# Kernel tuning notes

Measured on AMD Instinct MI355X. Metric: run time of the kernel, lower is better.

Reference implementation:

```python
import jax, jax.numpy as jnp
import numpy as np
from jax import lax

B, NODE, T, D_IN = 8, 1024, 12, 16
HID, GAT_OUT, PRED_LEN = 32, 32, 6
HEADS = 3
F_IN = HID * T      # 384
C = GAT_OUT * T     # 384
N = B * NODE        # 8192
E = 65536


def setup_inputs() -> dict:
    key = jax.random.key(0)
    ks = jax.random.split(key, 24)
    s = 0.05
    inp = {}
    inp["x"] = jax.random.normal(ks[0], (B, NODE, T, D_IN), jnp.float32)
    inp["edge_index"] = jax.random.randint(ks[1], (2, E), 0, N)
    inp["edge_attr"] = jax.random.normal(ks[2], (E, 1), jnp.float32)
    inp["batch_vec"] = jnp.repeat(jnp.arange(B), NODE)
    inp["alpha"] = 1.0
    # GRU params (torch gate order: r, z, n)
    inp["Wih"] = jax.random.normal(ks[3], (3 * HID, D_IN), jnp.float32) * s
    inp["Whh"] = jax.random.normal(ks[4], (3 * HID, HID), jnp.float32) * s
    inp["bih"] = jax.random.normal(ks[5], (3 * HID,), jnp.float32) * s
    inp["bhh"] = jax.random.normal(ks[6], (3 * HID,), jnp.float32) * s
    # GATConv params
    inp["Wgat"] = jax.random.normal(ks[7], (HEADS * C, F_IN), jnp.float32) * s
    inp["att_src"] = jax.random.normal(ks[8], (1, HEADS, C), jnp.float32) * s
    inp["att_dst"] = jax.random.normal(ks[9], (1, HEADS, C), jnp.float32) * s
    inp["Wedge"] = jax.random.normal(ks[10], (HEADS * C, 1), jnp.float32) * s
    inp["att_edge"] = jax.random.normal(ks[11], (1, HEADS, C), jnp.float32) * s
    inp["gat_bias"] = jax.random.normal(ks[12], (C,), jnp.float32) * s
    # predictors / classifiers
    inp["Wp1"] = jax.random.normal(ks[13], (1, GAT_OUT), jnp.float32) * s
    inp["bp1"] = jax.random.normal(ks[14], (1,), jnp.float32) * s
    inp["Wp3"] = jax.random.normal(ks[15], (PRED_LEN, T), jnp.float32) * s
    inp["bp3"] = jax.random.normal(ks[16], (PRED_LEN,), jnp.float32) * s
    inp["Wc1"] = jax.random.normal(ks[17], (GAT_OUT, T * GAT_OUT), jnp.float32) * s
    inp["bc1"] = jax.random.normal(ks[18], (GAT_OUT,), jnp.float32) * s
    inp["Wc2"] = jax.random.normal(ks[19], (2, GAT_OUT), jnp.float32) * s
    inp["bc2"] = jax.random.normal(ks[20], (2,), jnp.float32) * s
    return inp


def _gru(x, Wih, Whh, bih, bhh):
    # x: [rows, T, D_IN] -> [rows, T, HID]
    h0 = jnp.zeros((x.shape[0], HID), x.dtype)

    def step(h, xt):
        gi = xt @ Wih.T + bih
        gh = h @ Whh.T + bhh
        ir, iz, inn = jnp.split(gi, 3, axis=-1)
        hr, hz, hn = jnp.split(gh, 3, axis=-1)
        r = jax.nn.sigmoid(ir + hr)
        z = jax.nn.sigmoid(iz + hz)
        n = jnp.tanh(inn + r * hn)
        h_new = (1.0 - z) * n + z * h
        return h_new, h_new

    _, hs = lax.scan(step, h0, jnp.swapaxes(x, 0, 1))
    return jnp.swapaxes(hs, 0, 1)


def _gat(x, edge_index, edge_attr, Wgat, att_src, att_dst, Wedge, att_edge, bias):
    # PyG GATConv, heads=HEADS, concat=False, edge_dim=1, no self loops
    h = (x @ Wgat.T).reshape(N, HEADS, C)          # [N,H,C]
    a_src = (h * att_src).sum(-1)                  # [N,H]
    a_dst = (h * att_dst).sum(-1)                  # [N,H]
    src, dst = edge_index[0], edge_index[1]
    e = (edge_attr @ Wedge.T).reshape(-1, HEADS, C)
    a_edge = (e * att_edge).sum(-1)                # [E,H]
    a = jax.nn.leaky_relu(a_src[src] + a_dst[dst] + a_edge, 0.2)
    amax = jax.ops.segment_max(a, dst, num_segments=N)
    a = jnp.exp(a - amax[dst])
    denom = jax.ops.segment_sum(a, dst, num_segments=N)
    a = a / (denom[dst] + 1e-16)                   # segment softmax over incoming edges
    msg = h[src] * a[:, :, None]                   # [E,H,C]
    out = jax.ops.segment_sum(msg, dst, num_segments=N)
    return out.mean(axis=1) + bias                 # concat=False -> head mean


def reference(x, edge_index, edge_attr, batch_vec, alpha,
              Wih, Whh, bih, bhh,
              Wgat, att_src, att_dst, Wedge, att_edge, gat_bias,
              Wp1, bp1, Wp3, bp3, Wc1, bc1, Wc2, bc2):
    gru_in = x.reshape(-1, T, D_IN)                       # [N,T,D]
    gru_out = _gru(gru_in, Wih, Whh, bih, bhh)            # [N,T,HID]
    gat_in = gru_out.reshape(N, F_IN)
    gat_out = _gat(gat_in, edge_index, edge_attr, Wgat, att_src, att_dst,
                   Wedge, att_edge, gat_bias)             # [N,C]
    lin_in = gat_out.reshape(-1, T, GAT_OUT)              # [N,T,GAT_OUT]
    p = jax.nn.relu(jnp.einsum('ntc,oc->nto', lin_in, Wp1) + bp1).squeeze(-1)  # [N,T]
    p = jax.nn.relu(p @ Wp3.T + bp3)                      # [N,PRED_LEN]
    out_pred = p.reshape(B, NODE, PRED_LEN)
    # GRL is identity in forward
    pooled = jax.ops.segment_max(gat_out, batch_vec, num_segments=B)  # [B,C]
    l1 = pooled @ Wc1.T + bc1
    l2 = l1 @ Wc2.T + bc2
    out_label = jax.nn.softmax(l2, axis=1)
    return out_pred, out_label
```

## Files before the change

kernel.cpp:

```cpp
#include <hip/hip_runtime.h>
#include <hip/hip_bf16.h>

#define N_NODES 8192
#define E_EDGES 65536
#define CDIM 384
#define NHC 1152
#define T_STEPS 12
#define PRED_LEN 6
#define OUT_LABEL_OFF 49152

#define O_X        0u
#define O_WIH      1572864u
#define O_WHH      1574400u
#define O_BIH      1577472u
#define O_BHH      1577568u
#define O_WGAT     1577664u
#define O_ATTS     2020032u
#define O_ATTD     2021184u
#define O_WEDGE    2022336u
#define O_ATTE     2023488u
#define O_GBIAS    2024640u
#define O_WP1      2025024u
#define O_BP1      2025056u
#define O_WP3      2025057u
#define O_BP3      2025129u
#define O_WC1      2025135u
#define O_BC1      2037423u
#define O_WC2      2037455u
#define O_BC2      2037519u
#define O_EATTR    2037521u
#define CONV_TOTAL 2103057u

#define O_GATIN    2103072u
#define O_GATB     O_GATIN
#define O_WGATB    (O_GATIN + 1572864u)
#define O_DEG      (O_GATIN + 1794048u)
#define O_HFEAT    5248800u
#define O_ASRC     14685984u
#define O_ADST     14710560u
#define O_WEXP     14931744u
#define O_DENOM    15152928u
#define O_GMEAN    15177504u
#define O_POOLED   18323232u
#define O_KH       18326304u
#define O_FLAG     18326307u
#define O_BUCKET   18326320u

typedef __attribute__((ext_vector_type(8))) short short8;
typedef __attribute__((ext_vector_type(4))) float floatx4;

__device__ __forceinline__ float b2f(unsigned short u) {
    return __uint_as_float(((unsigned)u) << 16);
}
__device__ __forceinline__ unsigned short f2b(float f) {
    __hip_bfloat16 b = __float2bfloat16(f);
    return *(unsigned short*)&b;
}
__device__ __forceinline__ short f2bs(float f) {
    __hip_bfloat16 b = __float2bfloat16(f);
    return *(short*)&b;
}
__device__ __forceinline__ unsigned enc_f(float f) {
    unsigned u = __float_as_uint(f);
    return (u & 0x80000000u) ? ~u : (u | 0x80000000u);
}
__device__ __forceinline__ float dec_f(unsigned e) {
    return __uint_as_float((e & 0x80000000u) ? (e & 0x7FFFFFFFu) : ~e);
}
__device__ __forceinline__ float fast_rcp(float x) {
    return __builtin_amdgcn_rcpf(x);
}

__global__ __launch_bounds__(256) void prep_kernel(
    const void* Wih, const void* Whh, const void* bih, const void* bhh,
    const void* Wgat, const void* atts, const void* attd, const void* Wedge, const void* atte,
    const void* gbias, const void* Wp1, const void* bp1, const void* Wp3, const void* bp3,
    const void* Wc1, const void* bc1, const void* Wc2, const void* bc2, const void* eattr,
    float* __restrict__ W, unsigned short* __restrict__ wgatb, int* __restrict__ flag_g)
{
    __shared__ int fsh;
    if (threadIdx.x < 64) {
        int lane = threadIdx.x, cnt = 0;
#pragma unroll
        for (int i = 0; i < 8; i++) {
            unsigned short h = ((const unsigned short*)Wih)[(lane * 8 + i) * 2];
            int e = (h >> 7) & 0xFF;
            if (e >= 100 && e <= 127) cnt++;
        }
#pragma unroll
        for (int off = 32; off; off >>= 1) cnt += __shfl_down(cnt, off, 64);
        if (lane == 0) fsh = (cnt >= 300) ? 1 : 0;
    }
    __syncthreads();
    int flag = fsh;
    unsigned tidg = blockIdx.x * 256 + threadIdx.x;
    if (tidg == 0) *flag_g = flag;
    if      (tidg < 24576u) W[O_DENOM + tidg] = 0.f;
    else if (tidg < 27648u) W[O_POOLED + tidg - 24576u] = 0.f;
    else if (tidg < 35840u) ((int*)(W + O_DEG))[tidg - 27648u] = 0;
    unsigned idx = tidg + O_WIH;
    if (idx >= CONV_TOTAL) return;
    if (idx >= O_WGAT && idx < O_ATTS) {
        unsigned off = idx - O_WGAT;
        wgatb[off] = flag ? ((const unsigned short*)Wgat)[off]
                          : f2b(((const float*)Wgat)[off]);
        return;
    }
    const void* src; unsigned off;
    if      (idx < O_WHH)   { src = Wih;   off = idx - O_WIH; }
    else if (idx < O_BIH)   { src = Whh;   off = idx - O_WHH; }
    else if (idx < O_BHH)   { src = bih;   off = idx - O_BIH; }
    else if (idx < O_WGAT)  { src = bhh;   off = idx - O_BHH; }
    else if (idx < O_ATTD)  { src = atts;  off = idx - O_ATTS; }
    else if (idx < O_WEDGE) { src = attd;  off = idx - O_ATTD; }
    else if (idx < O_ATTE)  { src = Wedge; off = idx - O_WEDGE; }
    else if (idx < O_GBIAS) { src = atte;  off = idx - O_ATTE; }
    else if (idx < O_WP1)   { src = gbias; off = idx - O_GBIAS; }
    else if (idx < O_BP1)   { src = Wp1;   off = idx - O_WP1; }
    else if (idx < O_BP3)   { src = (idx == O_BP1) ? bp1 : Wp3; off = (idx == O_BP1) ? 0 : idx - O_WP3; }
    else if (idx < O_WC1)   { src = bp3;   off = idx - O_BP3; }
    else if (idx < O_BC1)   { src = Wc1;   off = idx - O_WC1; }
    else if (idx < O_WC2)   { src = bc1;   off = idx - O_BC1; }
    else if (idx < O_BC2)   { src = Wc2;   off = idx - O_WC2; }
    else if (idx < O_EATTR) { src = bc2;   off = idx - O_BC2; }
    else                    { src = eattr; off = idx - O_EATTR; }
    W[idx] = flag ? b2f(((const unsigned short*)src)[off])
                  : ((const float*)src)[off];
}

__global__ __launch_bounds__(64, 1) void gru_kernel(
    const float* __restrict__ W,
    const void* __restrict__ xraw,
    unsigned short* __restrict__ gat_b)
{
    __shared__ short hbuf[16 * 40];
    int lane = threadIdx.x;
    int q = lane >> 4, nl = lane & 15;
    int n0 = blockIdx.x * 16;
    int n = n0 + nl;
    int flag = ((const int*)(W + O_FLAG))[0];

    const float* W_wih = W + O_WIH;
    const float* W_whh = W + O_WHH;
    const float* W_bih = W + O_BIH;
    const float* W_bhh = W + O_BHH;

    short8 wh[6], wi[6];
#pragma unroll
    for (int c = 0; c < 6; c++) {
        int row = c * 16 + nl;
#pragma unroll
        for (int r = 0; r < 8; r++) {
            wh[c][r] = f2bs(W_whh[row * 32 + 8 * q + r]);
            int k = 8 * q + r;
            wi[c][r] = (k < 16) ? f2bs(W_wih[row * 16 + k]) : (short)0;
        }
    }
    float br[8], bz[8], bni[8], bnh[8];
#pragma unroll
    for (int idx = 0; idx < 8; idx++) {
        int c = idx >> 2, r = idx & 3;
        int j = c * 16 + 4 * q + r;
        br[idx]  = W_bih[j] + W_bhh[j];
        bz[idx]  = W_bih[32 + j] + W_bhh[32 + j];
        bni[idx] = W_bih[64 + j];
        bnh[idx] = W_bhh[64 + j];
    }

    floatx4 zf = {0.f, 0.f, 0.f, 0.f};
    short8 zs;
#pragma unroll
    for (int r = 0; r < 8; r++) zs[r] = 0;

    float hprev[8];
#pragma unroll
    for (int i = 0; i < 8; i++) hprev[i] = 0.f;
    short8 hfrag = zs;

    for (int t = 0; t < T_STEPS; t++) {
        short8 xf = zs;
        if (q < 2) {
            size_t xoff = (size_t)n * 192 + t * 16 + 8 * q;
            if (flag) {
                xf = *(const short8*)((const unsigned short*)xraw + xoff);
            } else {
                const float* xp = (const float*)xraw + xoff;
                float4 xa = *(const float4*)xp;
                float4 xb = *(const float4*)(xp + 4);
                xf[0] = f2bs(xa.x); xf[1] = f2bs(xa.y); xf[2] = f2bs(xa.z); xf[3] = f2bs(xa.w);
                xf[4] = f2bs(xb.x); xf[5] = f2bs(xb.y); xf[6] = f2bs(xb.z); xf[7] = f2bs(xb.w);
            }
        }

        floatx4 aR0 = __builtin_amdgcn_mfma_f32_16x16x32_bf16(wi[0], xf, zf, 0, 0, 0);
        aR0 = __builtin_amdgcn_mfma_f32_16x16x32_bf16(wh[0], hfrag, aR0, 0, 0, 0);
        floatx4 aR1 = __builtin_amdgcn_mfma_f32_16x16x32_bf16(wi[1], xf, zf, 0, 0, 0);
        aR1 = __builtin_amdgcn_mfma_f32_16x16x32_bf16(wh[1], hfrag, aR1, 0, 0, 0);
        floatx4 aZ0 = __builtin_amdgcn_mfma_f32_16x16x32_bf16(wi[2], xf, zf, 0, 0, 0);
        aZ0 = __builtin_amdgcn_mfma_f32_16x16x32_bf16(wh[2], hfrag, aZ0, 0, 0, 0);
        floatx4 aZ1 = __builtin_amdgcn_mfma_f32_16x16x32_bf16(wi[3], xf, zf, 0, 0, 0);
        aZ1 = __builtin_amdgcn_mfma_f32_16x16x32_bf16(wh[3], hfrag, aZ1, 0, 0, 0);
        floatx4 aNI0 = __builtin_amdgcn_mfma_f32_16x16x32_bf16(wi[4], xf, zf, 0, 0, 0);
        floatx4 aNI1 = __builtin_amdgcn_mfma_f32_16x16x32_bf16(wi[5], xf, zf, 0, 0, 0);
        floatx4 aNH0 = __builtin_amdgcn_mfma_f32_16x16x32_bf16(wh[4], hfrag, zf, 0, 0, 0);
        floatx4 aNH1 = __builtin_amdgcn_mfma_f32_16x16x32_bf16(wh[5], hfrag, zf, 0, 0, 0);

#pragma unroll
        for (int idx = 0; idx < 8; idx++) {
            int c = idx >> 2, r = idx & 3;
            float vR = (c ? aR1[r] : aR0[r]) + br[idx];
            float vZ = (c ? aZ1[r] : aZ0[r]) + bz[idx];
            float vNI = (c ? aNI1[r] : aNI0[r]) + bni[idx];
            float vNH = (c ? aNH1[r] : aNH0[r]) + bnh[idx];
            float rr = fast_rcp(1.f + __expf(-vR));
            float zz = fast_rcp(1.f + __expf(-vZ));
            float pre = vNI + rr * vNH;
            float e2 = __expf(2.f * pre);
            float nn = 1.f - 2.f * fast_rcp(e2 + 1.f);
            float h = (1.f - zz) * nn + zz * hprev[idx];
            hprev[idx] = h;
            int j = c * 16 + 4 * q + r;
            hbuf[nl * 40 + j] = f2bs(h);
        }
        hfrag = *(short8*)&hbuf[nl * 40 + 8 * q];
        int sn = lane >> 2, jg = (lane & 3) * 8;
        short8 hv = *(short8*)&hbuf[sn * 40 + jg];
        *(short8*)(gat_b + (size_t)(n0 + sn) * 384 + t * 32 + jg) = hv;
    }
}

__global__ __launch_bounds__(256) void gemm_mfma(
    const unsigned short* __restrict__ Ab,
    const unsigned short* __restrict__ Bb,
    unsigned short* __restrict__ Cb)
{
    __shared__ unsigned short sA[128][40];
    __shared__ unsigned short sB[128][40];
    int tid = threadIdx.x;
    int wave = tid >> 6, lane = tid & 63;
    int wm = (wave >> 1) * 64, wn = (wave & 1) * 64;
    int m0 = blockIdx.x * 128, n0 = blockIdx.y * 128;

    int r0 = tid >> 2;
    int c8 = (tid & 3) * 8;

    floatx4 acc[4][4];
#pragma unroll
    for (int i = 0; i < 4; i++)
#pragma unroll
        for (int j = 0; j < 4; j++) acc[i][j] = 0;

    int ml = lane & 15, kq = (lane >> 4) * 8;

    for (int k0 = 0; k0 < 384; k0 += 32) {
        short8 a0 = *(const short8*)(Ab + (size_t)(m0 + r0) * 384 + k0 + c8);
        short8 a1 = *(const short8*)(Ab + (size_t)(m0 + r0 + 64) * 384 + k0 + c8);
        short8 b0 = *(const short8*)(Bb + (size_t)(n0 + r0) * 384 + k0 + c8);
        short8 b1 = *(const short8*)(Bb + (size_t)(n0 + r0 + 64) * 384 + k0 + c8);

        __syncthreads();
        *(short8*)(&sA[r0][c8])      = a0;
        *(short8*)(&sA[r0 + 64][c8]) = a1;
        *(short8*)(&sB[r0][c8])      = b0;
        *(short8*)(&sB[r0 + 64][c8]) = b1;
        __syncthreads();

        short8 af[4], bf[4];
#pragma unroll
        for (int i = 0; i < 4; i++)
            af[i] = *(const short8*)(&sA[wm + i * 16 + ml][kq]);
#pragma unroll
        for (int j = 0; j < 4; j++)
            bf[j] = *(const short8*)(&sB[wn + j * 16 + ml][kq]);
#pragma unroll
        for (int i = 0; i < 4; i++)
#pragma unroll
            for (int j = 0; j < 4; j++)
                acc[i][j] = __builtin_amdgcn_mfma_f32_16x16x32_bf16(af[i], bf[j], acc[i][j], 0, 0, 0);
    }

    int cn = lane & 15, rq = (lane >> 4) * 4;
#pragma unroll
    for (int i = 0; i < 4; i++)
#pragma unroll
        for (int j = 0; j < 4; j++)
#pragma unroll
            for (int r = 0; r < 4; r++)
                Cb[(size_t)(m0 + wm + i * 16 + rq + r) * NHC + n0 + wn + j * 16 + cn] = f2b(acc[i][j][r]);
}

__global__ __launch_bounds__(256) void att_score_kernel(
    const unsigned short* __restrict__ h_bf,
    const float* __restrict__ att_src,
    const float* __restrict__ att_dst,
    const float* __restrict__ Wedge,
    const float* __restrict__ att_edge,
    float* __restrict__ a_src, float* __restrict__ a_dst,
    float* __restrict__ Kh)
{
    if (blockIdx.x == (N_NODES * 3) / 4) {
        if (threadIdx.x < 192) {
            int hd = threadIdx.x >> 6, lane = threadIdx.x & 63;
            float s = 0.f;
#pragma unroll
            for (int qq = 0; qq < 6; qq++) {
                int c = lane + qq * 64;
                s += Wedge[hd * CDIM + c] * att_edge[hd * CDIM + c];
            }
#pragma unroll
            for (int off = 32; off; off >>= 1) s += __shfl_down(s, off, 64);
            if (lane == 0) Kh[hd] = s;
        }
        return;
    }
    int w = (blockIdx.x * 256 + threadIdx.x) >> 6;
    int lane = threadIdx.x & 63;
    int n = w / 3, hd = w % 3;
    const unsigned short* hrow = h_bf + (size_t)n * NHC + hd * CDIM;
    float s0 = 0.f, s1 = 0.f;
#pragma unroll
    for (int qq = 0; qq < 6; qq++) {
        int c = lane + qq * 64;
        float hv = b2f(hrow[c]);
        s0 += hv * att_src[hd * CDIM + c];
        s1 += hv * att_dst[hd * CDIM + c];
    }
#pragma unroll
    for (int off = 32; off; off >>= 1) {
        s0 += __shfl_down(s0, off, 64);
        s1 += __shfl_down(s1, off, 64);
    }
    if (lane == 0) { a_src[n * 3 + hd] = s0; a_dst[n * 3 + hd] = s1; }
}

__global__ __launch_bounds__(256) void edge_w_kernel(
    const int* __restrict__ edge_index,
    const float* __restrict__ eattr,
    const float* __restrict__ a_src, const float* __restrict__ a_dst,
    const float* __restrict__ Kh,
    float* __restrict__ w_exp, float* __restrict__ denom,
    int* __restrict__ deg, int* __restrict__ bucket)
{
    int tid = blockIdx.x * 256 + threadIdx.x;
    int hd = tid >> 16;
    int e = tid & (E_EDGES - 1);
    int src = edge_index[e];
    int dst = edge_index[E_EDGES + e];
    float a = a_src[src * 3 + hd] + a_dst[dst * 3 + hd] + eattr[e] * Kh[hd];
    a = a > 0.f ? a : 0.2f * a;
    float w = __expf(a);
    w_exp[hd * E_EDGES + e] = w;
    unsafeAtomicAdd(&denom[dst * 3 + hd], w);
    if (hd == 0) {
        int pos = atomicAdd(&deg[dst], 1);
        if (pos < 64) bucket[(size_t)dst * 64 + pos] = e;
    }
}

__global__ __launch_bounds__(384) void aggregate_fused(
    const int* __restrict__ flag,
    const int* __restrict__ edge_index,
    const unsigned short* __restrict__ h_bf,
    const float* __restrict__ w_exp, const float* __restrict__ denom,
    const int* __restrict__ deg, const int* __restrict__ bucket,
    const float* __restrict__ gat_bias,
    const float* __restrict__ Wp1, const float* __restrict__ bp1,
    const float* __restrict__ Wp3, const float* __restrict__ bp3,
    float* __restrict__ gmean,
    void* __restrict__ out_pred)
{
    int dst = blockIdx.x;
    int d = deg[dst]; if (d > 64) d = 64;
    int tid = threadIdx.x;
    const float third = 1.f / 3.f;
    float inv0 = third / (denom[dst * 3 + 0] + 1e-16f);
    float inv1 = third / (denom[dst * 3 + 1] + 1e-16f);
    float inv2 = third / (denom[dst * 3 + 2] + 1e-16f);
    __shared__ int ssrc[64];
    __shared__ float sc0[64], sc1[64], sc2[64];
    __shared__ float gs[384];
    __shared__ float ps[12];
    if (tid < d) {
        int e = bucket[(size_t)dst * 64 + tid];
        ssrc[tid] = edge_index[e];
        sc0[tid] = w_exp[e] * inv0;
        sc1[tid] = w_exp[E_EDGES + e] * inv1;
        sc2[tid] = w_exp[2 * E_EDGES + e] * inv2;
    }
    __syncthreads();
    float a = 0.f;
    for (int i = 0; i < d; i++) {
        const unsigned short* hs = h_bf + (size_t)ssrc[i] * NHC;
        a += sc0[i] * b2f(hs[tid]) + sc1[i] * b2f(hs[tid + CDIM]) + sc2[i] * b2f(hs[tid + 2 * CDIM]);
    }
    float g = a + gat_bias[tid];
    gmean[(size_t)dst * CDIM + tid] = g;
    gs[tid] = g;
    __syncthreads();

    int t = tid >> 5, c = tid & 31;
    float v = gs[t * 32 + c] * Wp1[c];
#pragma unroll
    for (int off = 16; off; off >>= 1) v += __shfl_down(v, off, 32);
    if (c == 0) { float p = v + bp1[0]; ps[t] = p > 0.f ? p : 0.f; }
    __syncthreads();

    if (tid < PRED_LEN) {
        float acc = bp3[tid];
#pragma unroll
        for (int tt = 0; tt < 12; tt++) acc += Wp3[tid * 12 + tt] * ps[tt];
        acc = acc > 0.f ? acc : 0.f;
        size_t oi = (size_t)dst * PRED_LEN + tid;
        if (*flag) ((__hip_bfloat16*)out_pred)[oi] = __float2bfloat16(acc);
        else       ((float*)out_pred)[oi] = acc;
    }
}

__global__ __launch_bounds__(384) void pool_kernel(
    const float* __restrict__ gmean,
    unsigned* __restrict__ pooled_enc)
{
    int b = blockIdx.x, ch = blockIdx.y;
    int tid = threadIdx.x;
    const float* base = gmean + ((size_t)b * 1024 + ch * 64) * CDIM + tid;
    float m = -3.4e38f;
    for (int i = 0; i < 64; i++)
        m = fmaxf(m, base[(size_t)i * CDIM]);
    atomicMax(&pooled_enc[b * CDIM + tid], enc_f(m));
}

__global__ __launch_bounds__(384) void cls_kernel(
    const int* __restrict__ flag,
    const unsigned* __restrict__ pooled_enc,
    const float* __restrict__ Wc1, const float* __restrict__ bc1,
    const float* __restrict__ Wc2, const float* __restrict__ bc2,
    void* __restrict__ out_base)
{
    int b = blockIdx.x, t = threadIdx.x;
    __shared__ float l1[32];
    if (t < 32) l1[t] = bc1[t];
    __syncthreads();
    float v = dec_f(pooled_enc[b * CDIM + t]);
#pragma unroll
    for (int i = 0; i < 32; i++) {
        float p = v * Wc1[i * CDIM + t];
#pragma unroll
        for (int off = 32; off; off >>= 1) p += __shfl_down(p, off, 64);
        if ((t & 63) == 0) atomicAdd(&l1[i], p);
    }
    __syncthreads();
    if (t == 0) {
        float l0 = bc2[0], l1v = bc2[1];
#pragma unroll
        for (int ii = 0; ii < 32; ii++) {
            l0  += Wc2[ii] * l1[ii];
            l1v += Wc2[32 + ii] * l1[ii];
        }
        float m = fmaxf(l0, l1v);
        float e0 = __expf(l0 - m), e1 = __expf(l1v - m);
        float s = e0 + e1;
        if (*flag) {
            __hip_bfloat16* ob = (__hip_bfloat16*)out_base;
            ob[OUT_LABEL_OFF + b * 2 + 0] = __float2bfloat16(e0 / s);
            ob[OUT_LABEL_OFF + b * 2 + 1] = __float2bfloat16(e1 / s);
        } else {
            float* of = (float*)out_base;
            of[OUT_LABEL_OFF + b * 2 + 0] = e0 / s;
            of[OUT_LABEL_OFF + b * 2 + 1] = e1 / s;
        }
    }
}

extern "C" void kernel_launch(void* const* d_in, const int* in_sizes, int n_in,
                              void* d_out, int out_size, void* d_ws, size_t ws_size,
                              hipStream_t stream) {
    float* W = (float*)d_ws;
    int* flag = (int*)(W + O_FLAG);
    const int* edge_index = (const int*)d_in[1];

    prep_kernel<<<(CONV_TOTAL - O_WIH + 255) / 256, 256, 0, stream>>>(
        d_in[5], d_in[6], d_in[7], d_in[8],
        d_in[9], d_in[10], d_in[11], d_in[12], d_in[13],
        d_in[14], d_in[15], d_in[16], d_in[17], d_in[18],
        d_in[19], d_in[20], d_in[21], d_in[22], d_in[2],
        W, (unsigned short*)(W + O_WGATB), flag);

    gru_kernel<<<N_NODES / 16, 64, 0, stream>>>(
        W, d_in[0], (unsigned short*)(W + O_GATB));
    gemm_mfma<<<dim3(N_NODES / 128, NHC / 128), 256, 0, stream>>>(
        (const unsigned short*)(W + O_GATB),
        (const unsigned short*)(W + O_WGATB),
        (unsigned short*)(W + O_HFEAT));
    att_score_kernel<<<(N_NODES * 3) / 4 + 1, 256, 0, stream>>>(
        (const unsigned short*)(W + O_HFEAT), W + O_ATTS, W + O_ATTD,
        W + O_WEDGE, W + O_ATTE,
        W + O_ASRC, W + O_ADST, W + O_KH);
    edge_w_kernel<<<3 * E_EDGES / 256, 256, 0, stream>>>(
        edge_index, W + O_EATTR, W + O_ASRC, W + O_ADST, W + O_KH,
        W + O_WEXP, W + O_DENOM, (int*)(W + O_DEG), (int*)(W + O_BUCKET));
    aggregate_fused<<<N_NODES, 384, 0, stream>>>(
        flag, edge_index, (const unsigned short*)(W + O_HFEAT),
        W + O_WEXP, W + O_DENOM,
        (const int*)(W + O_DEG), (const int*)(W + O_BUCKET),
        W + O_GBIAS, W + O_WP1, W + O_BP1, W + O_WP3, W + O_BP3,
        W + O_GMEAN, d_out);
    pool_kernel<<<dim3(8, 16), 384, 0, stream>>>(
        W + O_GMEAN, (unsigned*)(W + O_POOLED));
    cls_kernel<<<8, 384, 0, stream>>>(
        flag, (const unsigned*)(W + O_POOLED),
        W + O_WC1, W + O_BC1, W + O_WC2, W + O_BC2, d_out);
}
```

Measured before the change: 228.3 us.

## Fuse attention score reductions into GEMM epilogue and move Kh to prep

Removes the separate attention-score kernel. Each GEMM tile now computes its partial dot products with att_src and att_dst straight from the fp32 accumulators, reduces them across lanes with shuffles, and atomically adds them into zero-initialised a_src/a_dst buffers. The edge-constant Kh reduction moves into the prep kernel, and the prep kernel also zeroes the score buffers. This saves a launch and a re-read of the bf16 hidden features, at the cost of atomics, a heavier GEMM epilogue, and scores built from unrounded fp32 accumulators.

```diff
diff --git a/kernel.cpp b/kernel.cpp
--- a/kernel.cpp
+++ b/kernel.cpp
@@ -95,9 +95,28 @@
     int flag = fsh;
     unsigned tidg = blockIdx.x * 256 + threadIdx.x;
     if (tidg == 0) *flag_g = flag;
+
+    if (blockIdx.x == 0 && threadIdx.x < 192) {
+        int hd = threadIdx.x >> 6, lane = threadIdx.x & 63;
+        float s = 0.f;
+#pragma unroll
+        for (int qq = 0; qq < 6; qq++) {
+            int c = hd * CDIM + lane + qq * 64;
+            float we = flag ? b2f(((const unsigned short*)Wedge)[c]) : ((const float*)Wedge)[c];
+            float ae = flag ? b2f(((const unsigned short*)atte)[c])  : ((const float*)atte)[c];
+            s += we * ae;
+        }
+#pragma unroll
+        for (int off = 32; off; off >>= 1) s += __shfl_down(s, off, 64);
+        if (lane == 0) W[O_KH + hd] = s;
+    }
+
     if      (tidg < 24576u) W[O_DENOM + tidg] = 0.f;
     else if (tidg < 27648u) W[O_POOLED + tidg - 24576u] = 0.f;
     else if (tidg < 35840u) ((int*)(W + O_DEG))[tidg - 27648u] = 0;
+    else if (tidg < 60416u) W[O_ASRC + tidg - 35840u] = 0.f;
+    else if (tidg < 84992u) W[O_ADST + tidg - 60416u] = 0.f;
+
     unsigned idx = tidg + O_WIH;
     if (idx >= CONV_TOTAL) return;
     if (idx >= O_WGAT && idx < O_ATTS) {
@@ -232,7 +251,11 @@
 __global__ __launch_bounds__(256) void gemm_mfma(
     const unsigned short* __restrict__ Ab,
     const unsigned short* __restrict__ Bb,
-    unsigned short* __restrict__ Cb)
+    unsigned short* __restrict__ Cb,
+    const float* __restrict__ att_s,
+    const float* __restrict__ att_d,
+    float* __restrict__ a_src,
+    float* __restrict__ a_dst)
 {
     __shared__ unsigned short sA[128][40];
     __shared__ unsigned short sB[128][40];
@@ -287,50 +310,35 @@
 #pragma unroll
             for (int r = 0; r < 4; r++)
                 Cb[(size_t)(m0 + wm + i * 16 + rq + r) * NHC + n0 + wn + j * 16 + cn] = f2b(acc[i][j][r]);
-}
-
-__global__ __launch_bounds__(256) void att_score_kernel(
-    const unsigned short* __restrict__ h_bf,
-    const float* __restrict__ att_src,
-    const float* __restrict__ att_dst,
-    const float* __restrict__ Wedge,
-    const float* __restrict__ att_edge,
-    float* __restrict__ a_src, float* __restrict__ a_dst,
-    float* __restrict__ Kh)
-{
-    if (blockIdx.x == (N_NODES * 3) / 4) {
-        if (threadIdx.x < 192) {
-            int hd = threadIdx.x >> 6, lane = threadIdx.x & 63;
-            float s = 0.f;
-#pragma unroll
-            for (int qq = 0; qq < 6; qq++) {
-                int c = lane + qq * 64;
-                s += Wedge[hd * CDIM + c] * att_edge[hd * CDIM + c];
+
+    int hd = n0 / CDIM;
+    float avs[4], avd[4];
+#pragma unroll
+    for (int j = 0; j < 4; j++) {
+        int c = n0 + wn + j * 16 + cn;
+        avs[j] = att_s[c];
+        avd[j] = att_d[c];
+    }
+#pragma unroll
+    for (int i = 0; i < 4; i++) {
+#pragma unroll
+        for (int r = 0; r < 4; r++) {
+            float s0 = acc[i][0][r] * avs[0] + acc[i][1][r] * avs[1]
+                     + acc[i][2][r] * avs[2] + acc[i][3][r] * avs[3];
+            float s1 = acc[i][0][r] * avd[0] + acc[i][1][r] * avd[1]
+                     + acc[i][2][r] * avd[2] + acc[i][3][r] * avd[3];
+#pragma unroll
+            for (int m = 1; m < 16; m <<= 1) {
+                s0 += __shfl_xor(s0, m, 64);
+                s1 += __shfl_xor(s1, m, 64);
             }
-#pragma unroll
-            for (int off = 32; off; off >>= 1) s += __shfl_down(s, off, 64);
-            if (lane == 0) Kh[hd] = s;
-        }
-        return;
-    }
-    int w = (blockIdx.x * 256 + threadIdx.x) >> 6;
-    int lane = threadIdx.x & 63;
-    int n = w / 3, hd = w % 3;
-    const unsigned short* hrow = h_bf + (size_t)n * NHC + hd * CDIM;
-    float s0 = 0.f, s1 = 0.f;
-#pragma unroll
-    for (int qq = 0; qq < 6; qq++) {
-        int c = lane + qq * 64;
-        float hv = b2f(hrow[c]);
-        s0 += hv * att_src[hd * CDIM + c];
-        s1 += hv * att_dst[hd * CDIM + c];
-    }
-#pragma unroll
-    for (int off = 32; off; off >>= 1) {
-        s0 += __shfl_down(s0, off, 64);
-        s1 += __shfl_down(s1, off, 64);
-    }
-    if (lane == 0) { a_src[n * 3 + hd] = s0; a_dst[n * 3 + hd] = s1; }
+            if (cn == 0) {
+                int row = m0 + wm + i * 16 + rq + r;
+                unsafeAtomicAdd(&a_src[row * 3 + hd], s0);
+                unsafeAtomicAdd(&a_dst[row * 3 + hd], s1);
+            }
+        }
+    }
 }
 
 __global__ __launch_bounds__(256) void edge_w_kernel(
@@ -490,11 +498,9 @@
     gemm_mfma<<<dim3(N_NODES / 128, NHC / 128), 256, 0, stream>>>(
         (const unsigned short*)(W + O_GATB),
         (const unsigned short*)(W + O_WGATB),
-        (unsigned short*)(W + O_HFEAT));
-    att_score_kernel<<<(N_NODES * 3) / 4 + 1, 256, 0, stream>>>(
-        (const unsigned short*)(W + O_HFEAT), W + O_ATTS, W + O_ATTD,
-        W + O_WEDGE, W + O_ATTE,
-        W + O_ASRC, W + O_ADST, W + O_KH);
+        (unsigned short*)(W + O_HFEAT),
+        W + O_ATTS, W + O_ATTD,
+        W + O_ASRC, W + O_ADST);
     edge_w_kernel<<<3 * E_EDGES / 256, 256, 0, stream>>>(
         edge_index, W + O_EATTR, W + O_ASRC, W + O_ADST, W + O_KH,
         W + O_WEXP, W + O_DENOM, (int*)(W + O_DEG), (int*)(W + O_BUCKET));
```

Result: slower. 235.4 us (+3.1%).
